# Kernel tuning notes

Measured on AMD Instinct MI355X. Metric: run time of the kernel, lower is better.

Reference implementation:

```python
import jax, jax.numpy as jnp
import numpy as np

B, Q, K, H = 8, 512, 512, 1024
NH, HD = 16, 64
MAX_REL = 512  # max_relative_positions


def setup_inputs() -> dict:
    key = jax.random.key(0)
    ks = jax.random.split(key, 16)
    s = 1.0 / np.sqrt(H)
    inp = {
        "query": jax.random.normal(ks[0], (B, Q, H), jnp.float32),
        "key": jax.random.normal(ks[1], (B, K, H), jnp.float32),
        "value": jax.random.normal(ks[2], (B, K, H), jnp.float32),
        "key_padding_mask": jax.random.randint(ks[3], (B, K), 0, 2, jnp.int32),
        "Wq": jax.random.normal(ks[4], (H, H), jnp.float32) * s,
        "bq": jnp.zeros((H,), jnp.float32),
        "Wk": jax.random.normal(ks[5], (H, H), jnp.float32) * s,
        "bk": jnp.zeros((H,), jnp.float32),
        "Wv": jax.random.normal(ks[6], (H, H), jnp.float32) * s,
        "bv": jnp.zeros((H,), jnp.float32),
        "Wo": jax.random.normal(ks[7], (H, H), jnp.float32) * s,
        "bo": jnp.zeros((H,), jnp.float32),
        "rel_table": jax.random.normal(ks[8], (2 * MAX_REL - 1, NH), jnp.float32) * 0.02,
        "local_bias": jax.random.normal(ks[9], (512, 512), jnp.float32) * 0.1,
        "log_scale": jnp.zeros((1,), jnp.float32),
        "attention_bias": jnp.zeros((1,), jnp.float32),
    }
    return inp


def reference(query, key, value, key_padding_mask, Wq, bq, Wk, bk, Wv, bv, Wo, bo,
              rel_table, local_bias, log_scale, attention_bias):
    # projections -> [B, NH, len, HD]
    q = (query @ Wq + bq).reshape(B, Q, NH, HD).transpose(0, 2, 1, 3)
    k = (key @ Wk + bk).reshape(B, K, NH, HD).transpose(0, 2, 1, 3)
    v = (value @ Wv + bv).reshape(B, K, NH, HD).transpose(0, 2, 1, 3)

    scores = jnp.einsum('bhqd,bhkd->bhqk', q, k) / jnp.sqrt(jnp.float32(HD))

    # relative position bias
    rel = jnp.arange(Q)[:, None] - jnp.arange(K)[None, :]
    bucket = jnp.clip(rel, -(MAX_REL - 1), MAX_REL - 1) + (MAX_REL - 1)
    rel_bias = rel_table[bucket]            # [Q, K, NH]
    scores = scores + rel_bias.transpose(2, 0, 1)[None]  # [1, NH, Q, K]

    # local bias (Q,K <= 512)
    scores = scores + local_bias[:Q, :K][None, None] * 0.05

    scale = jnp.clip(jnp.exp(log_scale), 1.0, 4.0)
    scores = scores * scale + attention_bias

    pad = (key_padding_mask == 0)[:, None, None, :]  # [B,1,1,K]
    scores = jnp.where(pad, -jnp.inf, scores)
    # clamp AFTER masking: -inf -> -50 (padded keys get tiny but nonzero weight)
    scores = jnp.clip(scores, -50.0, 50.0)

    attn = jax.nn.softmax(scores, axis=-1)
    out = jnp.einsum('bhqk,bhkd->bhqd', attn, v)
    out = out.transpose(0, 2, 1, 3).reshape(B, Q, H)
    out = out @ Wo + bo
    return out, attn
```

## Files before the change

### kernel.cpp

```cpp
#include <hip/hip_runtime.h>

#define B_ 8
#define LQ 512
#define LK 512
#define HDIM 1024
#define NH_ 16
#define HD_ 64

typedef unsigned short u16;
typedef __attribute__((ext_vector_type(4))) float f32x4;
typedef __attribute__((ext_vector_type(4))) int i32x4;
typedef __attribute__((ext_vector_type(8))) __bf16 bf16x8;

static __device__ __forceinline__ u16 f2bf(float f) {
    union { float f; unsigned u; } v; v.f = f;
    unsigned u = v.u;
    return (u16)((u + 0x7fffu + ((u >> 16) & 1u)) >> 16);
}

static __device__ __forceinline__ void gload_lds16(const u16* g, u16* l) {
    __builtin_amdgcn_global_load_lds((const __attribute__((address_space(1))) unsigned*)g,
                                     (__attribute__((address_space(3))) unsigned*)l, 16, 0, 0);
}

__global__ __launch_bounds__(256) void xcast_kernel(
    const float* __restrict__ x0, const float* __restrict__ x1, const float* __restrict__ x2,
    u16* __restrict__ o0, u16* __restrict__ o1, u16* __restrict__ o2)
{
    const float* X; u16* O;
    switch (blockIdx.z) { case 0: X = x0; O = o0; break; case 1: X = x1; O = o1; break;
                          default: X = x2; O = o2; }
    int i = blockIdx.x * 256 + threadIdx.x;
    f32x4 v = ((const f32x4*)X)[i];
    union { u16 u[4]; unsigned long long ull; } p;
    p.u[0] = f2bf(v[0]); p.u[1] = f2bf(v[1]); p.u[2] = f2bf(v[2]); p.u[3] = f2bf(v[3]);
    ((unsigned long long*)O)[i] = p.ull;
}

__global__ void wcast_kernel(const float* __restrict__ w0, const float* __restrict__ w1,
                             const float* __restrict__ w2, const float* __restrict__ w3,
                             u16* __restrict__ o0, u16* __restrict__ o1,
                             u16* __restrict__ o2, u16* __restrict__ o3) {
    const float* W; u16* O;
    switch (blockIdx.z) { case 0: W = w0; O = o0; break; case 1: W = w1; O = o1; break;
                          case 2: W = w2; O = o2; break; default: W = w3; O = o3; }
    __shared__ float t[32][33];
    int tx = threadIdx.x, ty = threadIdx.y;
    int n0 = blockIdx.x * 32, k0 = blockIdx.y * 32;
#pragma unroll
    for (int i = 0; i < 4; i++) {
        int k = ty * 4 + i;
        t[k][tx] = W[(k0 + k) * HDIM + n0 + tx];
    }
    __syncthreads();
#pragma unroll
    for (int i = 0; i < 4; i++) {
        int n = ty * 4 + i;
        O[(n0 + n) * HDIM + k0 + tx] = f2bf(t[tx][n]);
    }
}

__global__ __launch_bounds__(256) void proj2_kernel(
    const u16* __restrict__ x0, const u16* __restrict__ x1, const u16* __restrict__ x2,
    const u16* __restrict__ wt0, const u16* __restrict__ wt1, const u16* __restrict__ wt2,
    const float* __restrict__ bi0, const float* __restrict__ bi1, const float* __restrict__ bi2,
    u16* __restrict__ ot0, u16* __restrict__ ot1, u16* __restrict__ ot2)
{
    __shared__ u16 As[128 * 64];
    __shared__ u16 Bs[128 * 64];
    int bid = blockIdx.x;
    int swz = (bid & 7) * 96 + (bid >> 3);
    int z = swz >> 8, rem = swz & 255;
    int Mb = (rem >> 3) * 128, Nb = (rem & 7) * 128;
    const u16* X; const u16* WT; const float* bias; u16* out;
    switch (z) {
        case 0: X = x0; WT = wt0; bias = bi0; out = ot0; break;
        case 1: X = x1; WT = wt1; bias = bi1; out = ot1; break;
        default: X = x2; WT = wt2; bias = bi2; out = ot2; break;
    }
    int tid = threadIdx.x, lane = tid & 63, w = tid >> 6;
    int wm = (w & 1) * 64, wn = (w >> 1) * 64;
    int r16 = lane & 15, kg = lane >> 4;
    int rsw = (r16 & 7) * 8;
    int srow = lane >> 3;
    int scol = 8 * ((lane & 7) ^ (lane >> 3));
    const u16* gA = X + (size_t)Mb * HDIM;
    const u16* gB = WT + (size_t)Nb * HDIM;

    f32x4 acc[4][4] = {};
    for (int k0 = 0; k0 < HDIM; k0 += 64) {
#pragma unroll
        for (int i = 0; i < 4; i++) {
            int c = w * 4 + i;
            int row = c * 8 + srow;
            gload_lds16(&gA[(size_t)row * HDIM + k0 + scol], &As[c * 512]);
            gload_lds16(&gB[(size_t)row * HDIM + k0 + scol], &Bs[c * 512]);
        }
        __syncthreads();
#pragma unroll
        for (int kk = 0; kk < 2; kk++) {
            int colp = (kk * 32 + kg * 8) ^ rsw;
            bf16x8 a[4], b[4];
#pragma unroll
            for (int mt = 0; mt < 4; mt++) a[mt] = *(const bf16x8*)&As[(wm + mt * 16 + r16) * 64 + colp];
#pragma unroll
            for (int nt = 0; nt < 4; nt++) b[nt] = *(const bf16x8*)&Bs[(wn + nt * 16 + r16) * 64 + colp];
#pragma unroll
            for (int mt = 0; mt < 4; mt++)
#pragma unroll
                for (int nt = 0; nt < 4; nt++)
                    acc[mt][nt] = __builtin_amdgcn_mfma_f32_16x16x32_bf16(a[mt], b[nt], acc[mt][nt], 0, 0, 0);
        }
        __syncthreads();
    }
    int cr = (lane >> 4) * 4, cc = lane & 15;
#pragma unroll
    for (int nt = 0; nt < 4; nt++) {
        int n = Nb + wn + nt * 16 + cc;
        float bv = bias[n];
        int h = n >> 6, d = n & 63;
#pragma unroll
        for (int mt = 0; mt < 4; mt++) {
#pragma unroll
            for (int j = 0; j < 4; j++) {
                int m = Mb + wm + mt * 16 + cr + j;
                int b = m >> 9, l = m & 511;
                out[(((b * NH_ + h) * LQ) + l) * HD_ + d] = f2bf(acc[mt][nt][j] + bv);
            }
        }
    }
}

__global__ void vtrans_kernel(const u16* __restrict__ vb, u16* __restrict__ vT) {
    int bh = blockIdx.z;
    int k0 = blockIdx.x * 32, d0 = blockIdx.y * 32;
    __shared__ u16 t[32][33];
    int tx = threadIdx.x, ty = threadIdx.y;
    const u16* src = vb + (size_t)bh * (LK * HD_);
    u16* dst = vT + (size_t)bh * (LK * HD_);
#pragma unroll
    for (int i = 0; i < 4; i++) {
        int k = ty * 4 + i;
        t[k][tx] = src[(k0 + k) * HD_ + d0 + tx];
    }
    __syncthreads();
#pragma unroll
    for (int i = 0; i < 4; i++) {
        int d = ty * 4 + i;
        dst[(d0 + d) * LK + k0 + tx] = t[tx][d];
    }
}

__global__ __launch_bounds__(512) void attn2_kernel(
    const u16* __restrict__ qb, const u16* __restrict__ kb, const u16* __restrict__ vT,
    const int* __restrict__ kpm, const float* __restrict__ rel_table,
    const float* __restrict__ local_bias, const float* __restrict__ log_scale,
    const float* __restrict__ att_bias, float* __restrict__ attn_out, u16* __restrict__ ctx)
{
    __shared__ u16 Qs[32][72];
    __shared__ float rel_l[1024];
    __shared__ int pmask[512];
    __shared__ float red[2][32][8];
    __shared__ u16 P[32][520];
    __shared__ float pred[4][32][16];

    int bh = blockIdx.y;
    int q0 = blockIdx.x * 32;
    int b = bh >> 4, h = bh & 15;
    int tid = threadIdx.x, lane = tid & 63, w = tid >> 6;
    int r16 = lane & 15, kg = lane >> 4;

    float scale = fminf(fmaxf(__expf(log_scale[0]), 1.0f), 4.0f);
    float abias = att_bias[0];

    if (tid < 256) {
        int row = tid >> 3, c8 = tid & 7;
        *(i32x4*)&Qs[row][c8 * 8] = *(const i32x4*)&qb[((size_t)bh * LQ + q0 + row) * HD_ + c8 * 8];
    }
    for (int i = tid; i < 1023; i += 512) rel_l[i] = rel_table[i * NH_ + h];
    pmask[tid & 511] = kpm[b * LK + (tid & 511)];
    __syncthreads();

    bf16x8 aq[2][2];
#pragma unroll
    for (int m = 0; m < 2; m++)
#pragma unroll
        for (int kk = 0; kk < 2; kk++)
            aq[m][kk] = *(const bf16x8*)&Qs[m * 16 + r16][kk * 32 + kg * 8];

    f32x4 acc[2][4] = {};
    const u16* kbase = kb + ((size_t)bh * LK + w * 64) * HD_;
#pragma unroll
    for (int nt = 0; nt < 4; nt++) {
        bf16x8 bk0 = *(const bf16x8*)&kbase[(nt * 16 + r16) * HD_ + kg * 8];
        bf16x8 bk1 = *(const bf16x8*)&kbase[(nt * 16 + r16) * HD_ + 32 + kg * 8];
#pragma unroll
        for (int m = 0; m < 2; m++) {
            acc[m][nt] = __builtin_amdgcn_mfma_f32_16x16x32_bf16(aq[m][0], bk0, acc[m][nt], 0, 0, 0);
            acc[m][nt] = __builtin_amdgcn_mfma_f32_16x16x32_bf16(aq[m][1], bk1, acc[m][nt], 0, 0, 0);
        }
    }

    float rm[2][4];
#pragma unroll
    for (int m = 0; m < 2; m++)
#pragma unroll
        for (int j = 0; j < 4; j++) rm[m][j] = -1e30f;
#pragma unroll
    for (int m = 0; m < 2; m++) {
#pragma unroll
        for (int nt = 0; nt < 4; nt++) {
            int ki = w * 64 + nt * 16 + r16;
            bool masked = (pmask[ki] == 0);
#pragma unroll
            for (int j = 0; j < 4; j++) {
                int row = m * 16 + kg * 4 + j;
                int qi = q0 + row;
                float s = acc[m][nt][j] * 0.125f;
                s += rel_l[qi - ki + 511];
                s += local_bias[qi * LK + ki] * 0.05f;
                s = s * scale + abias;
                s = masked ? -50.0f : fminf(fmaxf(s, -50.0f), 50.0f);
                acc[m][nt][j] = s;
                rm[m][j] = fmaxf(rm[m][j], s);
            }
        }
    }
#pragma unroll
    for (int m = 0; m < 2; m++)
#pragma unroll
        for (int j = 0; j < 4; j++) {
            float v = rm[m][j];
            v = fmaxf(v, __shfl_xor(v, 1));
            v = fmaxf(v, __shfl_xor(v, 2));
            v = fmaxf(v, __shfl_xor(v, 4));
            v = fmaxf(v, __shfl_xor(v, 8));
            rm[m][j] = v;
        }
    if (r16 == 0) {
#pragma unroll
        for (int m = 0; m < 2; m++)
#pragma unroll
            for (int j = 0; j < 4; j++) red[0][m * 16 + kg * 4 + j][w] = rm[m][j];
    }
    __syncthreads();
    float fm[2][4];
#pragma unroll
    for (int m = 0; m < 2; m++)
#pragma unroll
        for (int j = 0; j < 4; j++) {
            int row = m * 16 + kg * 4 + j;
            float v = red[0][row][0];
#pragma unroll
            for (int ww = 1; ww < 8; ww++) v = fmaxf(v, red[0][row][ww]);
            fm[m][j] = v;
        }
    float ps[2][4] = {};
#pragma unroll
    for (int m = 0; m < 2; m++)
#pragma unroll
        for (int nt = 0; nt < 4; nt++)
#pragma unroll
            for (int j = 0; j < 4; j++) {
                float e = __expf(acc[m][nt][j] - fm[m][j]);
                acc[m][nt][j] = e;
                ps[m][j] += e;
            }
#pragma unroll
    for (int m = 0; m < 2; m++)
#pragma unroll
        for (int j = 0; j < 4; j++) {
            float v = ps[m][j];
            v += __shfl_xor(v, 1);
            v += __shfl_xor(v, 2);
            v += __shfl_xor(v, 4);
            v += __shfl_xor(v, 8);
            ps[m][j] = v;
        }
    if (r16 == 0) {
#pragma unroll
        for (int m = 0; m < 2; m++)
#pragma unroll
            for (int j = 0; j < 4; j++) red[1][m * 16 + kg * 4 + j][w] = ps[m][j];
    }
    __syncthreads();

    float* dst = attn_out + ((size_t)bh * LQ + q0) * (size_t)LK + w * 64;
#pragma unroll
    for (int m = 0; m < 2; m++)
#pragma unroll
        for (int j = 0; j < 4; j++) {
            int row = m * 16 + kg * 4 + j;
            float sum = 0.f;
#pragma unroll
            for (int ww = 0; ww < 8; ww++) sum += red[1][row][ww];
            float inv = 1.0f / sum;
#pragma unroll
            for (int nt = 0; nt < 4; nt++) {
                float p = acc[m][nt][j] * inv;
                dst[(size_t)row * LK + nt * 16 + r16] = p;
                P[row][w * 64 + nt * 16 + r16] = f2bf(p);
            }
        }
    __syncthreads();

    int wd = (w & 3) * 16;
    int kh = (w >> 2) * 256;
    const u16* vbase = vT + (size_t)bh * (HD_ * LK);
    f32x4 po[2] = {};
#pragma unroll
    for (int kt = 0; kt < 8; kt++) {
        int k0 = kh + kt * 32;
        bf16x8 bvf = *(const bf16x8*)&vbase[(size_t)(wd + r16) * LK + k0 + kg * 8];
#pragma unroll
        for (int m = 0; m < 2; m++) {
            bf16x8 af = *(const bf16x8*)&P[m * 16 + r16][k0 + kg * 8];
            po[m] = __builtin_amdgcn_mfma_f32_16x16x32_bf16(af, bvf, po[m], 0, 0, 0);
        }
    }
    if (w >= 4) {
#pragma unroll
        for (int m = 0; m < 2; m++)
#pragma unroll
            for (int j = 0; j < 4; j++)
                pred[w & 3][m * 16 + kg * 4 + j][r16] = po[m][j];
    }
    __syncthreads();
    if (w < 4) {
#pragma unroll
        for (int m = 0; m < 2; m++)
#pragma unroll
            for (int j = 0; j < 4; j++) {
                int row = m * 16 + kg * 4 + j;
                float v = po[m][j] + pred[w][row][r16];
                ctx[((size_t)(b * LQ + q0 + row)) * HDIM + h * HD_ + wd + r16] = f2bf(v);
            }
    }
}

__global__ __launch_bounds__(256) void oproj2_kernel(
    const u16* __restrict__ ctx, const u16* __restrict__ WT,
    const float* __restrict__ bias, float* __restrict__ out)
{
    __shared__ u16 As[128 * 64];
    __shared__ u16 Bs[128 * 64];
    int bid = blockIdx.x;
    int idx = (bid & 7) * 32 + (bid >> 3);
    int Mb = (idx >> 3) * 128, Nb = (idx & 7) * 128;
    int tid = threadIdx.x, lane = tid & 63, w = tid >> 6;
    int wm = (w & 1) * 64, wn = (w >> 1) * 64;
    int r16 = lane & 15, kg = lane >> 4;
    int rsw = (r16 & 7) * 8;
    int srow = lane >> 3;
    int scol = 8 * ((lane & 7) ^ (lane >> 3));
    const u16* gA = ctx + (size_t)Mb * HDIM;
    const u16* gB = WT + (size_t)Nb * HDIM;

    f32x4 acc[4][4] = {};
    for (int k0 = 0; k0 < HDIM; k0 += 64) {
#pragma unroll
        for (int i = 0; i < 4; i++) {
            int c = w * 4 + i;
            int row = c * 8 + srow;
            gload_lds16(&gA[(size_t)row * HDIM + k0 + scol], &As[c * 512]);
            gload_lds16(&gB[(size_t)row * HDIM + k0 + scol], &Bs[c * 512]);
        }
        __syncthreads();
#pragma unroll
        for (int kk = 0; kk < 2; kk++) {
            int colp = (kk * 32 + kg * 8) ^ rsw;
            bf16x8 a[4], b[4];
#pragma unroll
            for (int mt = 0; mt < 4; mt++) a[mt] = *(const bf16x8*)&As[(wm + mt * 16 + r16) * 64 + colp];
#pragma unroll
            for (int nt = 0; nt < 4; nt++) b[nt] = *(const bf16x8*)&Bs[(wn + nt * 16 + r16) * 64 + colp];
#pragma unroll
            for (int mt = 0; mt < 4; mt++)
#pragma unroll
                for (int nt = 0; nt < 4; nt++)
                    acc[mt][nt] = __builtin_amdgcn_mfma_f32_16x16x32_bf16(a[mt], b[nt], acc[mt][nt], 0, 0, 0);
        }
        __syncthreads();
    }
    int cr = (lane >> 4) * 4, cc = lane & 15;
#pragma unroll
    for (int nt = 0; nt < 4; nt++) {
        int n = Nb + wn + nt * 16 + cc;
        float bv = bias[n];
#pragma unroll
        for (int mt = 0; mt < 4; mt++) {
#pragma unroll
            for (int j = 0; j < 4; j++) {
                int m = Mb + wm + mt * 16 + cr + j;
                out[(size_t)m * HDIM + n] = acc[mt][nt][j] + bv;
            }
        }
    }
}

extern "C" void kernel_launch(void* const* d_in, const int* in_sizes, int n_in,
                              void* d_out, int out_size, void* d_ws, size_t ws_size,
                              hipStream_t stream) {
    (void)in_sizes; (void)n_in; (void)out_size; (void)ws_size;
    const float* query = (const float*)d_in[0];
    const float* key_  = (const float*)d_in[1];
    const float* value = (const float*)d_in[2];
    const int*   kpm   = (const int*)d_in[3];
    const float* Wq = (const float*)d_in[4];  const float* bq = (const float*)d_in[5];
    const float* Wk = (const float*)d_in[6];  const float* bk = (const float*)d_in[7];
    const float* Wv = (const float*)d_in[8];  const float* bv = (const float*)d_in[9];
    const float* Wo = (const float*)d_in[10]; const float* bo = (const float*)d_in[11];
    const float* rel_table  = (const float*)d_in[12];
    const float* local_bias = (const float*)d_in[13];
    const float* log_scale  = (const float*)d_in[14];
    const float* att_bias   = (const float*)d_in[15];

    char* ws = (char*)d_ws;
    u16* WTq = (u16*)(ws + 0ull);
    u16* WTk = (u16*)(ws + (2ull << 20));
    u16* WTv = (u16*)(ws + (4ull << 20));
    u16* WTo = (u16*)(ws + (6ull << 20));
    u16* qb  = (u16*)(ws + (8ull << 20));
    u16* kb  = (u16*)(ws + (16ull << 20));
    u16* vb  = (u16*)(ws + (24ull << 20));
    u16* vT  = (u16*)(ws + (32ull << 20));
    u16* ctx = (u16*)(ws + (40ull << 20));
    u16* xq  = (u16*)(ws + (32ull << 20));
    u16* xk  = (u16*)(ws + (40ull << 20));
    u16* xv  = (u16*)(ws + (48ull << 20));

    float* out  = (float*)d_out;
    float* attn = out + (size_t)4096 * 1024;

    xcast_kernel<<<dim3(4096, 1, 3), 256, 0, stream>>>(query, key_, value, xq, xk, xv);
    wcast_kernel<<<dim3(32, 32, 4), dim3(32, 8), 0, stream>>>(Wq, Wk, Wv, Wo, WTq, WTk, WTv, WTo);
    proj2_kernel<<<768, 256, 0, stream>>>(xq, xk, xv, WTq, WTk, WTv, bq, bk, bv, qb, kb, vb);
    vtrans_kernel<<<dim3(16, 2, 128), dim3(32, 8), 0, stream>>>(vb, vT);
    attn2_kernel<<<dim3(16, 128), 512, 0, stream>>>(qb, kb, vT, kpm, rel_table, local_bias,
                                                    log_scale, att_bias, attn, ctx);
    oproj2_kernel<<<256, 256, 0, stream>>>(ctx, WTo, bo, out);
}
```

Before: 182.2 us.

## Precompute combined relative and local bias table in bf16 before attention

Adds a prep kernel that folds the relative-position bias, scaled local bias, scale and additive bias into a per-head bf16 table. The attention kernel then does one fused multiply-add per score instead of an LDS gather plus an fp32 global load. This halves the bias bytes read and removes the rel_table staging. Attention-probability stores become nontemporal. It costs an extra launch, an 8 MB table write, and bf16 rounding of the bias.

```diff
diff --git a/kernel.cpp b/kernel.cpp
--- a/kernel.cpp
+++ b/kernel.cpp
@@ -16,6 +16,11 @@
     union { float f; unsigned u; } v; v.f = f;
     unsigned u = v.u;
     return (u16)((u + 0x7fffu + ((u >> 16) & 1u)) >> 16);
+}
+
+static __device__ __forceinline__ float bf2f(u16 u) {
+    union { unsigned u; float f; } v; v.u = ((unsigned)u) << 16;
+    return v.f;
 }
 
 static __device__ __forceinline__ void gload_lds16(const u16* g, u16* l) {
@@ -58,6 +63,29 @@
         int n = ty * 4 + i;
         O[(n0 + n) * HDIM + k0 + tx] = f2bf(t[tx][n]);
     }
+}
+
+__global__ __launch_bounds__(256) void biasprep_kernel(
+    const float* __restrict__ rel_table, const float* __restrict__ local_bias,
+    const float* __restrict__ log_scale, const float* __restrict__ att_bias,
+    u16* __restrict__ Tb)
+{
+    int idx = blockIdx.x * 256 + threadIdx.x;
+    int base = idx * 8;
+    int h = base >> 18;
+    int rem = base & 262143;
+    int qi = rem >> 9, ki0 = rem & 511;
+    float scale = fminf(fmaxf(__expf(log_scale[0]), 1.0f), 4.0f);
+    float ab = att_bias[0];
+    union { u16 u[8]; i32x4 v; } o;
+#pragma unroll
+    for (int t = 0; t < 8; t++) {
+        int ki = ki0 + t;
+        float r = rel_table[(qi - ki + 511) * NH_ + h];
+        float lb = local_bias[qi * 512 + ki];
+        o.u[t] = f2bf((r + lb * 0.05f) * scale + ab);
+    }
+    *(i32x4*)&Tb[base] = o.v;
 }
 
 __global__ __launch_bounds__(256) void proj2_kernel(
@@ -153,12 +181,11 @@
 
 __global__ __launch_bounds__(512) void attn2_kernel(
     const u16* __restrict__ qb, const u16* __restrict__ kb, const u16* __restrict__ vT,
-    const int* __restrict__ kpm, const float* __restrict__ rel_table,
-    const float* __restrict__ local_bias, const float* __restrict__ log_scale,
-    const float* __restrict__ att_bias, float* __restrict__ attn_out, u16* __restrict__ ctx)
+    const int* __restrict__ kpm, const u16* __restrict__ Tb,
+    const float* __restrict__ log_scale,
+    float* __restrict__ attn_out, u16* __restrict__ ctx)
 {
     __shared__ u16 Qs[32][72];
-    __shared__ float rel_l[1024];
     __shared__ int pmask[512];
     __shared__ float red[2][32][8];
     __shared__ u16 P[32][520];
@@ -170,14 +197,12 @@
     int tid = threadIdx.x, lane = tid & 63, w = tid >> 6;
     int r16 = lane & 15, kg = lane >> 4;
 
-    float scale = fminf(fmaxf(__expf(log_scale[0]), 1.0f), 4.0f);
-    float abias = att_bias[0];
+    float cscale = 0.125f * fminf(fmaxf(__expf(log_scale[0]), 1.0f), 4.0f);
 
     if (tid < 256) {
         int row = tid >> 3, c8 = tid & 7;
         *(i32x4*)&Qs[row][c8 * 8] = *(const i32x4*)&qb[((size_t)bh * LQ + q0 + row) * HD_ + c8 * 8];
     }
-    for (int i = tid; i < 1023; i += 512) rel_l[i] = rel_table[i * NH_ + h];
     pmask[tid & 511] = kpm[b * LK + (tid & 511)];
     __syncthreads();
 
@@ -201,6 +226,7 @@
         }
     }
 
+    const u16* Th = Tb + ((size_t)h << 18);
     float rm[2][4];
 #pragma unroll
     for (int m = 0; m < 2; m++)
@@ -216,11 +242,9 @@
             for (int j = 0; j < 4; j++) {
                 int row = m * 16 + kg * 4 + j;
                 int qi = q0 + row;
-                float s = acc[m][nt][j] * 0.125f;
-                s += rel_l[qi - ki + 511];
-                s += local_bias[qi * LK + ki] * 0.05f;
-                s = s * scale + abias;
-                s = masked ? -50.0f : fminf(fmaxf(s, -50.0f), 50.0f);
+                float s = fmaf(acc[m][nt][j], cscale, bf2f(Th[qi * 512 + ki]));
+                s = fminf(fmaxf(s, -50.0f), 50.0f);
+                s = masked ? -50.0f : s;
                 acc[m][nt][j] = s;
                 rm[m][j] = fmaxf(rm[m][j], s);
             }
@@ -298,7 +322,7 @@
 #pragma unroll
             for (int nt = 0; nt < 4; nt++) {
                 float p = acc[m][nt][j] * inv;
-                dst[(size_t)row * LK + nt * 16 + r16] = p;
+                __builtin_nontemporal_store(p, &dst[(size_t)row * LK + nt * 16 + r16]);
                 P[row][w * 64 + nt * 16 + r16] = f2bf(p);
             }
         }
@@ -428,6 +452,7 @@
     u16* xq  = (u16*)(ws + (32ull << 20));
     u16* xk  = (u16*)(ws + (40ull << 20));
     u16* xv  = (u16*)(ws + (48ull << 20));
+    u16* Tb  = (u16*)(ws + (48ull << 20));
 
     float* out  = (float*)d_out;
     float* attn = out + (size_t)4096 * 1024;
@@ -436,7 +461,7 @@
     wcast_kernel<<<dim3(32, 32, 4), dim3(32, 8), 0, stream>>>(Wq, Wk, Wv, Wo, WTq, WTk, WTv, WTo);
     proj2_kernel<<<768, 256, 0, stream>>>(xq, xk, xv, WTq, WTk, WTv, bq, bk, bv, qb, kb, vb);
     vtrans_kernel<<<dim3(16, 2, 128), dim3(32, 8), 0, stream>>>(vb, vT);
-    attn2_kernel<<<dim3(16, 128), 512, 0, stream>>>(qb, kb, vT, kpm, rel_table, local_bias,
-                                                    log_scale, att_bias, attn, ctx);
+    biasprep_kernel<<<2048, 256, 0, stream>>>(rel_table, local_bias, log_scale, att_bias, Tb);
+    attn2_kernel<<<dim3(16, 128), 512, 0, stream>>>(qb, kb, vT, kpm, Tb, log_scale, attn, ctx);
     oproj2_kernel<<<256, 256, 0, stream>>>(ctx, WTo, bo, out);
 }
```

Result: faster. 167.8 us (-7.9%).
